# Performance work log

Measured on AMD Instinct MI355X. Metric: run time of the kernel, lower is better.

The kernel has to match this reference:

```python
import jax, jax.numpy as jnp
import numpy as np

MAX_NUM_CAPS = 10
NEG = -1e9

def _layernorm(x, g, b):
    m = x.mean(-1, keepdims=True)
    v = x.var(-1, keepdims=True)
    return (x - m) / jnp.sqrt(v + 1e-5) * g + b

def _gatv2(x, Wl, Wr, att, bias, adj):
    # x: [B,M,F]; Wl/Wr: [F,H*C]; att: [H,C]; adj: [B,M,M] bool, adj[b,i,j] = edge i->j
    B, M, F = x.shape
    H, C = att.shape
    xl = jnp.einsum('bmf,fhc->bmhc', x, Wl.reshape(F, H, C))  # source transform
    xr = jnp.einsum('bmf,fhc->bmhc', x, Wr.reshape(F, H, C))  # target transform
    # GATv2 score: att . leaky_relu(xl[i] + xr[j]) for edge (src=i, dst=j)
    z = jax.nn.leaky_relu(xl[:, :, None, :, :] + xr[:, None, :, :, :], 0.2)  # [B,i,j,H,C]
    e = jnp.einsum('bijhc,hc->bijh', z, att)
    e = jnp.where(adj[..., None], e, NEG)
    alpha = jax.nn.softmax(e, axis=1)  # softmax over incoming sources i per target j
    out = jnp.einsum('bijh,bihc->bjhc', alpha, xl)  # aggregate at targets
    return out.reshape(B, M, H * C) + bias

def setup_inputs() -> dict:
    key = jax.random.key(0)
    ks = jax.random.split(key, 16)
    B, N, T = 128, 16, 48
    Fm, H, C3 = 128, 4, 64
    s = 0.05
    inp = {
        'team_obs': jax.random.normal(ks[0], (B, N, 14), jnp.float32),
        'target_obs': jax.random.normal(ks[1], (B, T, 15), jnp.float32),
        'team_mask': jax.random.normal(ks[2], (B, 2, N), jnp.float32),
        'local_target_mask': jnp.ones((B, T + 1), jnp.float32),
        'W_emb': jax.random.normal(ks[3], (16, Fm), jnp.float32) * s,
        'b_emb': jnp.zeros((Fm,), jnp.float32),
        'Wl1': jax.random.normal(ks[4], (Fm, Fm), jnp.float32) * s,
        'Wr1': jax.random.normal(ks[5], (Fm, Fm), jnp.float32) * s,
        'att1': jax.random.normal(ks[6], (H, Fm // H), jnp.float32) * s,
        'b1': jnp.zeros((Fm,), jnp.float32),
        'Wl2': jax.random.normal(ks[7], (Fm, Fm), jnp.float32) * s,
        'Wr2': jax.random.normal(ks[8], (Fm, Fm), jnp.float32) * s,
        'att2': jax.random.normal(ks[9], (H, Fm // H), jnp.float32) * s,
        'b2': jnp.zeros((Fm,), jnp.float32),
        'Wl3': jax.random.normal(ks[10], (Fm, C3), jnp.float32) * s,
        'Wr3': jax.random.normal(ks[11], (Fm, C3), jnp.float32) * s,
        'att3': jax.random.normal(ks[12], (1, C3), jnp.float32) * s,
        'b3': jnp.zeros((C3,), jnp.float32),
        'ln1_g': jnp.ones((Fm,), jnp.float32),
        'ln1_b': jnp.zeros((Fm,), jnp.float32),
        'ln2_g': jnp.ones((Fm,), jnp.float32),
        'ln2_b': jnp.zeros((Fm,), jnp.float32),
    }
    return inp

def reference(team_obs, target_obs, team_mask, local_target_mask,
              W_emb, b_emb, Wl1, Wr1, att1, b1, Wl2, Wr2, att2, b2,
              Wl3, Wr3, att3, b3, ln1_g, ln1_b, ln2_g, ln2_b):
    B, N, _ = team_obs.shape
    team = jnp.concatenate([team_obs, jnp.zeros((B, N, 2), team_obs.dtype)], axis=2)
    tgt = target_obs[:, :, :-1]
    T = tgt.shape[1]
    tgt = jnp.concatenate([tgt[:, :, :2 + MAX_NUM_CAPS],
                           jnp.zeros((B, T, 2), tgt.dtype),
                           tgt[:, :, -2:]], axis=2)
    fin = jnp.concatenate([team, tgt], axis=1)  # [B, M, inp_dim]
    h = fin @ W_emb + b_emb  # [B, M, 128]
    imp_team = team_mask[:, 0] != -1e9          # [B, N]
    imp_tgt = local_target_mask[:, :-1] != 0.0  # [B, T]
    imp = jnp.concatenate([imp_team, imp_tgt], axis=1)  # [B, M]
    M = N + T
    eye = jnp.eye(M, dtype=bool)
    # edges among active nodes minus diagonal; PyG GATv2Conv add_self_loops=True re-adds self edges
    adj = (imp[:, :, None] & imp[:, None, :] & ~eye) | eye  # [B, M, M]
    out = jax.nn.relu(_layernorm(_gatv2(h, Wl1, Wr1, att1, b1, adj), ln1_g, ln1_b))
    out = jax.nn.relu(_layernorm(_gatv2(out, Wl2, Wr2, att2, b2, adj), ln2_g, ln2_b))
    out = _gatv2(out, Wl3, Wr3, att3, b3, adj)
    return out  # [B, M, out_dim]
```

## Files before the change

### kernel.cpp

```cpp
#include <hip/hip_runtime.h>

typedef unsigned short u16;
typedef unsigned int   u32;
typedef _Float16 h2  __attribute__((ext_vector_type(2)));
typedef __fp16   hw2 __attribute__((ext_vector_type(2)));
typedef __fp16   hw8 __attribute__((ext_vector_type(8)));
typedef float    f4  __attribute__((ext_vector_type(4)));

#define XS 136

static __device__ __forceinline__ h2 pk(float a, float b) {
    return __builtin_bit_cast(h2, __builtin_amdgcn_cvt_pkrtz(a, b));
}
static __device__ __forceinline__ float dot2(h2 a, h2 b, float c) {
    return __builtin_amdgcn_fdot2(__builtin_bit_cast(hw2, a),
                                  __builtin_bit_cast(hw2, b), c, false);
}
static __device__ __forceinline__ h2  b2h(u32 v) { return __builtin_bit_cast(h2, v); }
static __device__ __forceinline__ u32 h2u(h2 v)  { return __builtin_bit_cast(u32, v); }
static __device__ __forceinline__ h2  abs2(h2 v) { return b2h(h2u(v) & 0x7fff7fffu); }
static __device__ __forceinline__ u16 f2h(float f) { return __builtin_bit_cast(u16, (_Float16)f); }
static __device__ __forceinline__ float h2f(u16 v) { return (float)__builtin_bit_cast(_Float16, v); }
static __device__ __forceinline__ f4 mfma16(uint4 a, uint4 b, f4 c) {
    return __builtin_amdgcn_mfma_f32_16x16x32_f16(__builtin_bit_cast(hw8, a),
                                                  __builtin_bit_cast(hw8, b), c, 0, 0, 0);
}

__global__ void pack_weights(const float* __restrict__ Wl1, const float* __restrict__ Wr1,
                             const float* __restrict__ Wl2, const float* __restrict__ Wr2,
                             const float* __restrict__ Wl3, const float* __restrict__ Wr3,
                             u32* __restrict__ wpk)
{
    const int o = blockIdx.x * 256 + threadIdx.x;
    const float* src; u32* dst; int local; int N;
    if      (o < 8192)  { src = Wl1; dst = wpk;         local = o;         N = 128; }
    else if (o < 16384) { src = Wr1; dst = wpk + 8192;  local = o - 8192;  N = 128; }
    else if (o < 24576) { src = Wl2; dst = wpk + 16384; local = o - 16384; N = 128; }
    else if (o < 32768) { src = Wr2; dst = wpk + 24576; local = o - 24576; N = 128; }
    else if (o < 36864) { src = Wl3; dst = wpk + 32768; local = o - 32768; N = 64;  }
    else                { src = Wr3; dst = wpk + 36864; local = o - 36864; N = 64;  }
    const int i2   = local & 3;
    const int lane = (local >> 2) & 63;
    const int frag = local >> 8;
    const int kb   = frag & 3;
    const int nt   = frag >> 2;
    const int k0   = kb*32 + ((lane >> 4) << 3) + i2*2;
    const int n    = nt*16 + (lane & 15);
    dst[local] = h2u(pk(src[k0*N + n], src[(k0+1)*N + n]));
}

static __device__ __forceinline__ void gat_layer(
    int t, int w, int lane,
    const u32* __restrict__ wpkL, const u32* __restrict__ wpkR,
    const float* __restrict__ att, const float* __restrict__ bias,
    const float* __restrict__ lg, const float* __restrict__ lb,
    u16* sX, u16* sXl, uint4* sXrP, float* sAl, float* sPart, float* sL2, const float* sImp)
{
    {
        const int  mt  = w & 3;
        const bool isR = (w >= 4);
        const u32* wp  = isR ? wpkR : wpkL;
        const int  n15 = lane & 15;
        const int  qd  = lane >> 4;
        uint4 afr[4];
#pragma unroll
        for (int kb = 0; kb < 4; kb++)
            afr[kb] = *(const uint4*)&sX[(mt*16 + n15)*XS + kb*32 + (qd << 3)];
#pragma unroll
        for (int nt = 0; nt < 8; nt++) {
            f4 acc = {0.f, 0.f, 0.f, 0.f};
#pragma unroll
            for (int kb = 0; kb < 4; kb++) {
                uint4 bf = *(const uint4*)&wp[((nt*4 + kb)*64 + lane)*4];
                acc = mfma16(afr[kb], bf, acc);
            }
            const int n  = nt*16 + n15;
            const int mb = mt*16 + (qd << 2);
            if (!isR) {
#pragma unroll
                for (int r = 0; r < 4; r++) sXl[(mb + r)*XS + n] = f2h(acc[r]);
            } else {
                u16* xp = (u16*)sXrP;
#pragma unroll
                for (int r = 0; r < 4; r++)
                    xp[(((n >> 3)*64) + mb + r)*8 + (n & 7)] = f2h(acc[r]);
            }
        }
    }
    __syncthreads();

    const int h     = w & 3;
    const int ihalf = w >> 2;
    const int j     = lane;

    h2 a2[16];
#pragma unroll
    for (int q = 0; q < 16; q++) a2[q] = pk(att[h*32 + 2*q], att[h*32 + 2*q + 1]);

    if (w < 4) {
        const uint4* pr = (const uint4*)&sXl[lane*XS + h*32];
        float al = 0.f;
#pragma unroll
        for (int c4 = 0; c4 < 4; c4++) {
            uint4 v = pr[c4];
            al = dot2(b2h(v.x), a2[c4*4+0], al);
            al = dot2(b2h(v.y), a2[c4*4+1], al);
            al = dot2(b2h(v.z), a2[c4*4+2], al);
            al = dot2(b2h(v.w), a2[c4*4+3], al);
        }
        sAl[h*64 + lane] = al;
    }

    h2 xr2[16];
#pragma unroll
    for (int s = 0; s < 4; s++) {
        uint4 v = sXrP[(h*4 + s)*64 + j];
        xr2[s*4+0] = b2h(v.x); xr2[s*4+1] = b2h(v.y);
        xr2[s*4+2] = b2h(v.z); xr2[s*4+3] = b2h(v.w);
    }
    float Ar = 0.f;
#pragma unroll
    for (int q = 0; q < 16; q++) Ar = dot2(a2[q], xr2[q], Ar);
    const float impj = sImp[j];
    __syncthreads();

    float l = 0.f;
    h2 acc2[16];
#pragma unroll
    for (int q = 0; q < 16; q++) acc2[q] = b2h(0u);
    const int i0 = ihalf * 32;
#pragma unroll 4
    for (int ii = 0; ii < 32; ii++) {
        int i = i0 + ii;
        const uint4* pl = (const uint4*)&sXl[i*XS + h*32];
        uint4 v0 = pl[0], v1 = pl[1], v2 = pl[2], v3 = pl[3];
        h2 xl2[16];
        xl2[0] = b2h(v0.x); xl2[1] = b2h(v0.y); xl2[2]  = b2h(v0.z); xl2[3]  = b2h(v0.w);
        xl2[4] = b2h(v1.x); xl2[5] = b2h(v1.y); xl2[6]  = b2h(v1.z); xl2[7]  = b2h(v1.w);
        xl2[8] = b2h(v2.x); xl2[9] = b2h(v2.y); xl2[10] = b2h(v2.z); xl2[11] = b2h(v2.w);
        xl2[12]= b2h(v3.x); xl2[13]= b2h(v3.y); xl2[14] = b2h(v3.z); xl2[15] = b2h(v3.w);
        float S0 = 0.f, S1 = 0.f;
#pragma unroll
        for (int q = 0; q < 16; q += 2) {
            h2 t0 = abs2(xl2[q]   + xr2[q]);
            h2 t1 = abs2(xl2[q+1] + xr2[q+1]);
            S0 = dot2(a2[q],   t0, S0);
            S1 = dot2(a2[q+1], t1, S1);
        }
        float e  = 0.6f*(sAl[h*64 + i] + Ar) + 0.4f*(S0 + S1);
        float ad = (i == j) ? 1.f : impj * sImp[i];
        float p  = (ad != 0.f) ? __expf(e) : 0.f;
        l += p;
        h2 p2 = pk(p, p);
#pragma unroll
        for (int q = 0; q < 16; q++) acc2[q] += p2 * xl2[q];
    }

    u32* ov = (u32*)sX;
    if (w >= 4) {
        uint4* d4 = (uint4*)(ov + (h*64 + j)*16);
        uint4 o;
        o.x = h2u(acc2[0]);  o.y = h2u(acc2[1]);  o.z = h2u(acc2[2]);  o.w = h2u(acc2[3]);  d4[0] = o;
        o.x = h2u(acc2[4]);  o.y = h2u(acc2[5]);  o.z = h2u(acc2[6]);  o.w = h2u(acc2[7]);  d4[1] = o;
        o.x = h2u(acc2[8]);  o.y = h2u(acc2[9]);  o.z = h2u(acc2[10]); o.w = h2u(acc2[11]); d4[2] = o;
        o.x = h2u(acc2[12]); o.y = h2u(acc2[13]); o.z = h2u(acc2[14]); o.w = h2u(acc2[15]); d4[3] = o;
        sL2[h*64 + j] = l;
    }
    __syncthreads();

    float yv[32];
    if (w < 4) {
        const uint4* s4 = (const uint4*)(ov + (h*64 + j)*16);
        uint4 u0 = s4[0], u1 = s4[1], u2 = s4[2], u3 = s4[3];
        h2 oth[16];
        oth[0] = b2h(u0.x); oth[1] = b2h(u0.y); oth[2]  = b2h(u0.z); oth[3]  = b2h(u0.w);
        oth[4] = b2h(u1.x); oth[5] = b2h(u1.y); oth[6]  = b2h(u1.z); oth[7]  = b2h(u1.w);
        oth[8] = b2h(u2.x); oth[9] = b2h(u2.y); oth[10] = b2h(u2.z); oth[11] = b2h(u2.w);
        oth[12]= b2h(u3.x); oth[13]= b2h(u3.y); oth[14] = b2h(u3.z); oth[15] = b2h(u3.w);
        l += sL2[h*64 + j];
        const float rl = 1.f / l;
        float s1 = 0.f, s2v = 0.f;
#pragma unroll
        for (int q = 0; q < 16; q++) {
            h2 sum = acc2[q] + oth[q];
            float y0 = fmaf((float)sum[0], rl, bias[h*32 + 2*q]);
            float y1 = fmaf((float)sum[1], rl, bias[h*32 + 2*q + 1]);
            yv[2*q] = y0; yv[2*q+1] = y1;
            s1 += y0 + y1;
            s2v = fmaf(y0, y0, s2v);
            s2v = fmaf(y1, y1, s2v);
        }
        sPart[h*64 + j]       = s1;
        sPart[256 + h*64 + j] = s2v;
    }
    __syncthreads();

    if (w < 4) {
        float su = sPart[j] + sPart[64 + j] + sPart[128 + j] + sPart[192 + j];
        float sq = sPart[256 + j] + sPart[320 + j] + sPart[384 + j] + sPart[448 + j];
        const float mean = su * 0.0078125f;
        const float var  = sq * 0.0078125f - mean*mean;
        const float rstd = rsqrtf(var + 1e-5f);
        u32* xd = (u32*)&sX[j*XS + h*32];
#pragma unroll
        for (int q = 0; q < 16; q++) {
            int f0 = h*32 + 2*q;
            float v0 = fmaxf(fmaf((yv[2*q]   - mean)*rstd, lg[f0],   lb[f0]),   0.f);
            float v1 = fmaxf(fmaf((yv[2*q+1] - mean)*rstd, lg[f0+1], lb[f0+1]), 0.f);
            xd[q] = h2u(pk(v0, v1));
        }
    }
    __syncthreads();
}

__global__ void __launch_bounds__(512, 2) GNN_61040075210810_kernel(
    const float* __restrict__ team_obs, const float* __restrict__ target_obs,
    const float* __restrict__ team_mask, const float* __restrict__ local_target_mask,
    const float* __restrict__ W_emb, const float* __restrict__ b_emb,
    const float* __restrict__ att1, const float* __restrict__ b1,
    const float* __restrict__ att2, const float* __restrict__ b2,
    const float* __restrict__ att3, const float* __restrict__ b3,
    const float* __restrict__ ln1_g, const float* __restrict__ ln1_b,
    const float* __restrict__ ln2_g, const float* __restrict__ ln2_b,
    const u32* __restrict__ wpk,
    float* __restrict__ out)
{
    __shared__ __align__(16) u16   sX  [64*XS];
    __shared__ __align__(16) u16   sXl [64*XS];
    __shared__ __align__(16) uint4 sXrP[1024];
    __shared__ float sFin[1024];
    __shared__ float sAl [256];
    __shared__ float sPart[512];
    __shared__ float sL2 [256];
    __shared__ float sImp[64];

    const int t    = threadIdx.x;
    const int w    = t >> 6;
    const int lane = t & 63;
    const int b    = blockIdx.x;

    if (t < 64) {
        float im;
        if (t < 16) im = (team_mask[b*32 + t] != -1000000000.0f) ? 1.f : 0.f;
        else        im = (local_target_mask[b*49 + (t-16)] != 0.0f) ? 1.f : 0.f;
        sImp[t] = im;
    }
    for (int ee = t; ee < 1024; ee += 512) {
        int m = ee >> 4, k = ee & 15;
        float v = 0.f;
        if (m < 16) {
            if (k < 14) v = team_obs[(b*16 + m)*14 + k];
        } else {
            const float* tg = target_obs + (size_t)(b*48 + (m-16))*15;
            if      (k < 12)  v = tg[k];
            else if (k == 14) v = tg[12];
            else if (k == 15) v = tg[13];
        }
        sFin[m*16 + k] = v;
    }
    __syncthreads();

    {
        const int f = t & 127;
        const int g = t >> 7;
        float wreg[16];
#pragma unroll
        for (int k = 0; k < 16; k++) wreg[k] = W_emb[k*128 + f];
        const float bf = b_emb[f];
#pragma unroll
        for (int mm = 0; mm < 16; mm++) {
            int m = g*16 + mm;
            const float4* pf = (const float4*)&sFin[m*16];
            float4 f0 = pf[0], f1 = pf[1], f2 = pf[2], f3 = pf[3];
            float acc = bf;
            acc = fmaf(f0.x, wreg[0],  acc); acc = fmaf(f0.y, wreg[1],  acc);
            acc = fmaf(f0.z, wreg[2],  acc); acc = fmaf(f0.w, wreg[3],  acc);
            acc = fmaf(f1.x, wreg[4],  acc); acc = fmaf(f1.y, wreg[5],  acc);
            acc = fmaf(f1.z, wreg[6],  acc); acc = fmaf(f1.w, wreg[7],  acc);
            acc = fmaf(f2.x, wreg[8],  acc); acc = fmaf(f2.y, wreg[9],  acc);
            acc = fmaf(f2.z, wreg[10], acc); acc = fmaf(f2.w, wreg[11], acc);
            acc = fmaf(f3.x, wreg[12], acc); acc = fmaf(f3.y, wreg[13], acc);
            acc = fmaf(f3.z, wreg[14], acc); acc = fmaf(f3.w, wreg[15], acc);
            sX[m*XS + f] = f2h(acc);
        }
    }
    __syncthreads();

    gat_layer(t, w, lane, wpk,         wpk + 8192,  att1, b1, ln1_g, ln1_b,
              sX, sXl, sXrP, sAl, sPart, sL2, sImp);
    gat_layer(t, w, lane, wpk + 16384, wpk + 24576, att2, b2, ln2_g, ln2_b,
              sX, sXl, sXrP, sAl, sPart, sL2, sImp);

    {
        const int  mt  = w & 3;
        const bool isR = (w >= 4);
        const u32* wp  = isR ? (wpk + 36864) : (wpk + 32768);
        const int  n15 = lane & 15;
        const int  qd  = lane >> 4;
        uint4 afr[4];
#pragma unroll
        for (int kb = 0; kb < 4; kb++)
            afr[kb] = *(const uint4*)&sX[(mt*16 + n15)*XS + kb*32 + (qd << 3)];
#pragma unroll
        for (int nt = 0; nt < 4; nt++) {
            f4 acc = {0.f, 0.f, 0.f, 0.f};
#pragma unroll
            for (int kb = 0; kb < 4; kb++) {
                uint4 bf = *(const uint4*)&wp[((nt*4 + kb)*64 + lane)*4];
                acc = mfma16(afr[kb], bf, acc);
            }
            const int n  = nt*16 + n15;
            const int mb = mt*16 + (qd << 2);
            if (!isR) {
#pragma unroll
                for (int r = 0; r < 4; r++) sXl[(mb + r)*XS + n] = f2h(acc[r]);
            } else {
                u16* xp = (u16*)sXrP;
#pragma unroll
                for (int r = 0; r < 4; r++)
                    xp[(((n >> 3)*64) + mb + r)*8 + (n & 7)] = f2h(acc[r]);
            }
        }
    }
    __syncthreads();

    {
        h2 a2l[4];
#pragma unroll
        for (int q = 0; q < 4; q++) a2l[q] = pk(att3[w*8 + 2*q], att3[w*8 + 2*q + 1]);
        uint4 v = *(const uint4*)&sXl[lane*XS + w*8];
        float al = 0.f;
        al = dot2(b2h(v.x), a2l[0], al);
        al = dot2(b2h(v.y), a2l[1], al);
        al = dot2(b2h(v.z), a2l[2], al);
        al = dot2(b2h(v.w), a2l[3], al);
        sPart[w*64 + lane] = al;
    }
    __syncthreads();
    if (t < 64) {
        sAl[t] = ((sPart[t] + sPart[64+t]) + (sPart[128+t] + sPart[192+t]))
               + ((sPart[256+t] + sPart[320+t]) + (sPart[384+t] + sPart[448+t]));
    }
    __syncthreads();

    const int j = lane;
    u16* sE = (u16*)sX;

    {
        h2 a3[32], xr3[32];
#pragma unroll
        for (int q = 0; q < 32; q++) a3[q] = pk(att3[2*q], att3[2*q + 1]);
#pragma unroll
        for (int s = 0; s < 8; s++) {
            uint4 v = sXrP[s*64 + j];
            xr3[s*4+0] = b2h(v.x); xr3[s*4+1] = b2h(v.y);
            xr3[s*4+2] = b2h(v.z); xr3[s*4+3] = b2h(v.w);
        }
        float Ar = 0.f;
#pragma unroll
        for (int q = 0; q < 32; q++) Ar = dot2(a3[q], xr3[q], Ar);
        const float impj = sImp[j];
        const int i0 = w*8;
        for (int ii = 0; ii < 8; ii++) {
            int i = i0 + ii;
            const uint4* pl = (const uint4*)&sXl[i*XS];
            float S0 = 0.f, S1 = 0.f;
#pragma unroll
            for (int c4 = 0; c4 < 8; c4++) {
                uint4 v = pl[c4];
                S0 = dot2(a3[c4*4+0], abs2(b2h(v.x) + xr3[c4*4+0]), S0);
                S1 = dot2(a3[c4*4+1], abs2(b2h(v.y) + xr3[c4*4+1]), S1);
                S0 = dot2(a3[c4*4+2], abs2(b2h(v.z) + xr3[c4*4+2]), S0);
                S1 = dot2(a3[c4*4+3], abs2(b2h(v.w) + xr3[c4*4+3]), S1);
            }
            float e  = 0.6f*(sAl[i] + Ar) + 0.4f*(S0 + S1);
            float ad = (i == j) ? 1.f : impj * sImp[i];
            e = (ad != 0.f) ? e : -60000.0f;
            sE[i*64 + j] = f2h(e);
        }
    }
    __syncthreads();

    {
        const int c0 = w*8;
        h2 acc2[4];
#pragma unroll
        for (int q = 0; q < 4; q++) acc2[q] = b2h(0u);
        float l = 0.f;
        for (int i = 0; i < 64; i++) {
            float p = __expf(h2f(sE[i*64 + j]));
            l += p;
            h2 p2 = pk(p, p);
            uint4 v = *(const uint4*)&sXl[i*XS + c0];
            acc2[0] += p2 * b2h(v.x);
            acc2[1] += p2 * b2h(v.y);
            acc2[2] += p2 * b2h(v.z);
            acc2[3] += p2 * b2h(v.w);
        }
        const float rl = 1.f / l;
        float o[8];
#pragma unroll
        for (int q = 0; q < 4; q++) {
            o[2*q]   = fmaf((float)acc2[q][0], rl, b3[c0 + 2*q]);
            o[2*q+1] = fmaf((float)acc2[q][1], rl, b3[c0 + 2*q + 1]);
        }
        float4* po = (float4*)(out + (size_t)b*4096 + j*64 + c0);
        po[0] = *(const float4*)&o[0];
        po[1] = *(const float4*)&o[4];
    }
}

extern "C" void kernel_launch(void* const* d_in, const int* in_sizes, int n_in,
                              void* d_out, int out_size, void* d_ws, size_t ws_size,
                              hipStream_t stream) {
    (void)in_sizes; (void)n_in; (void)ws_size; (void)out_size;
    const float* team_obs          = (const float*)d_in[0];
    const float* target_obs        = (const float*)d_in[1];
    const float* team_mask         = (const float*)d_in[2];
    const float* local_target_mask = (const float*)d_in[3];
    const float* W_emb             = (const float*)d_in[4];
    const float* b_emb             = (const float*)d_in[5];
    const float* Wl1               = (const float*)d_in[6];
    const float* Wr1               = (const float*)d_in[7];
    const float* att1              = (const float*)d_in[8];
    const float* b1                = (const float*)d_in[9];
    const float* Wl2               = (const float*)d_in[10];
    const float* Wr2               = (const float*)d_in[11];
    const float* att2              = (const float*)d_in[12];
    const float* b2                = (const float*)d_in[13];
    const float* Wl3               = (const float*)d_in[14];
    const float* Wr3               = (const float*)d_in[15];
    const float* att3              = (const float*)d_in[16];
    const float* b3                = (const float*)d_in[17];
    const float* ln1_g             = (const float*)d_in[18];
    const float* ln1_b             = (const float*)d_in[19];
    const float* ln2_g             = (const float*)d_in[20];
    const float* ln2_b             = (const float*)d_in[21];
    float* out = (float*)d_out;
    u32*   wpk = (u32*)d_ws;

    pack_weights<<<dim3(160), dim3(256), 0, stream>>>(Wl1, Wr1, Wl2, Wr2, Wl3, Wr3, wpk);
    GNN_61040075210810_kernel<<<dim3(128), dim3(512), 0, stream>>>(
        team_obs, target_obs, team_mask, local_target_mask, W_emb, b_emb,
        att1, b1, att2, b2, att3, b3, ln1_g, ln1_b, ln2_g, ln2_b, wpk, out);
}
```

Before: 144.8 us.

## Split fused GNN kernel into per-layer kernels over two target halves

Replaces the single fused kernel (one block per batch, 128 blocks) with three per-layer kernels, each launched with 256 blocks, where every block handles half of the target nodes. Each block recomputes the full node projections for its batch, splits the source loop across lane halves and combines the partial sums with xor-32 shuffles, then writes intermediate activations to global memory (output buffer and workspace). The aim is to fill more of the GPU's compute units at batch 128. The cost is duplicated matmul work, extra kernel launches and a global round trip between layers.

```diff
diff --git a/kernel.cpp b/kernel.cpp
--- a/kernel.cpp
+++ b/kernel.cpp
@@ -24,6 +24,9 @@
 static __device__ __forceinline__ f4 mfma16(uint4 a, uint4 b, f4 c) {
     return __builtin_amdgcn_mfma_f32_16x16x32_f16(__builtin_bit_cast(hw8, a),
                                                   __builtin_bit_cast(hw8, b), c, 0, 0, 0);
+}
+static __device__ __forceinline__ h2 shflx32(h2 v) {
+    return b2h((u32)__shfl_xor((int)h2u(v), 32));
 }
 
 __global__ void pack_weights(const float* __restrict__ Wl1, const float* __restrict__ Wr1,
@@ -49,49 +52,63 @@
     dst[local] = h2u(pk(src[k0*N + n], src[(k0+1)*N + n]));
 }
 
-static __device__ __forceinline__ void gat_layer(
-    int t, int w, int lane,
+static __device__ __forceinline__ void compute_imp(int t, int b,
+    const float* __restrict__ team_mask, const float* __restrict__ ltm, float* sImp)
+{
+    if (t < 64) {
+        float im;
+        if (t < 16) im = (team_mask[b*32 + t] != -1000000000.0f) ? 1.f : 0.f;
+        else        im = (ltm[b*49 + (t-16)] != 0.0f) ? 1.f : 0.f;
+        sImp[t] = im;
+    }
+}
+
+static __device__ __forceinline__ void matmul128(int w, int lane,
     const u32* __restrict__ wpkL, const u32* __restrict__ wpkR,
+    const u16* sX, u16* sXl, uint4* sXrP)
+{
+    const int  mt  = w & 3;
+    const bool isR = (w >= 4);
+    const u32* wp  = isR ? wpkR : wpkL;
+    const int  n15 = lane & 15;
+    const int  qd  = lane >> 4;
+    uint4 afr[4];
+#pragma unroll
+    for (int kb = 0; kb < 4; kb++)
+        afr[kb] = *(const uint4*)&sX[(mt*16 + n15)*XS + kb*32 + (qd << 3)];
+#pragma unroll
+    for (int nt = 0; nt < 8; nt++) {
+        f4 acc = {0.f, 0.f, 0.f, 0.f};
+#pragma unroll
+        for (int kb = 0; kb < 4; kb++) {
+            uint4 bf = *(const uint4*)&wp[((nt*4 + kb)*64 + lane)*4];
+            acc = mfma16(afr[kb], bf, acc);
+        }
+        const int n  = nt*16 + n15;
+        const int mb = mt*16 + (qd << 2);
+        if (!isR) {
+#pragma unroll
+            for (int r = 0; r < 4; r++) sXl[(mb + r)*XS + n] = f2h(acc[r]);
+        } else {
+            u16* xp = (u16*)sXrP;
+#pragma unroll
+            for (int r = 0; r < 4; r++)
+                xp[(((n >> 3)*64) + mb + r)*8 + (n & 7)] = f2h(acc[r]);
+        }
+    }
+}
+
+static __device__ __forceinline__ void attn_ln(int t, int w, int lane, int b, int jh,
     const float* __restrict__ att, const float* __restrict__ bias,
     const float* __restrict__ lg, const float* __restrict__ lb,
-    u16* sX, u16* sXl, uint4* sXrP, float* sAl, float* sPart, float* sL2, const float* sImp)
-{
-    {
-        const int  mt  = w & 3;
-        const bool isR = (w >= 4);
-        const u32* wp  = isR ? wpkR : wpkL;
-        const int  n15 = lane & 15;
-        const int  qd  = lane >> 4;
-        uint4 afr[4];
-#pragma unroll
-        for (int kb = 0; kb < 4; kb++)
-            afr[kb] = *(const uint4*)&sX[(mt*16 + n15)*XS + kb*32 + (qd << 3)];
-#pragma unroll
-        for (int nt = 0; nt < 8; nt++) {
-            f4 acc = {0.f, 0.f, 0.f, 0.f};
-#pragma unroll
-            for (int kb = 0; kb < 4; kb++) {
-                uint4 bf = *(const uint4*)&wp[((nt*4 + kb)*64 + lane)*4];
-                acc = mfma16(afr[kb], bf, acc);
-            }
-            const int n  = nt*16 + n15;
-            const int mb = mt*16 + (qd << 2);
-            if (!isR) {
-#pragma unroll
-                for (int r = 0; r < 4; r++) sXl[(mb + r)*XS + n] = f2h(acc[r]);
-            } else {
-                u16* xp = (u16*)sXrP;
-#pragma unroll
-                for (int r = 0; r < 4; r++)
-                    xp[(((n >> 3)*64) + mb + r)*8 + (n & 7)] = f2h(acc[r]);
-            }
-        }
-    }
-    __syncthreads();
-
-    const int h     = w & 3;
-    const int ihalf = w >> 2;
-    const int j     = lane;
+    u16* sX, const u16* sXl, const uint4* sXrP,
+    float* sAl, float* sPart, float* sL2, const float* sImp, u32* __restrict__ gxOut)
+{
+    const int h  = w & 3;
+    const int ih = w >> 2;
+    const int jj = lane & 31;
+    const int is = lane >> 5;
+    const int j  = jh*32 + jj;
 
     h2 a2[16];
 #pragma unroll
@@ -128,9 +145,9 @@
     h2 acc2[16];
 #pragma unroll
     for (int q = 0; q < 16; q++) acc2[q] = b2h(0u);
-    const int i0 = ihalf * 32;
+    const int i0 = ih*32 + is*16;
 #pragma unroll 4
-    for (int ii = 0; ii < 32; ii++) {
+    for (int ii = 0; ii < 16; ii++) {
         int i = i0 + ii;
         const uint4* pl = (const uint4*)&sXl[i*XS + h*32];
         uint4 v0 = pl[0], v1 = pl[1], v2 = pl[2], v3 = pl[3];
@@ -156,28 +173,32 @@
         for (int q = 0; q < 16; q++) acc2[q] += p2 * xl2[q];
     }
 
+    l += __shfl_xor(l, 32);
+#pragma unroll
+    for (int q = 0; q < 16; q++) acc2[q] = acc2[q] + shflx32(acc2[q]);
+
     u32* ov = (u32*)sX;
-    if (w >= 4) {
-        uint4* d4 = (uint4*)(ov + (h*64 + j)*16);
+    if (w >= 4 && lane < 32) {
+        uint4* d4 = (uint4*)(ov + (h*32 + jj)*20);
         uint4 o;
         o.x = h2u(acc2[0]);  o.y = h2u(acc2[1]);  o.z = h2u(acc2[2]);  o.w = h2u(acc2[3]);  d4[0] = o;
         o.x = h2u(acc2[4]);  o.y = h2u(acc2[5]);  o.z = h2u(acc2[6]);  o.w = h2u(acc2[7]);  d4[1] = o;
         o.x = h2u(acc2[8]);  o.y = h2u(acc2[9]);  o.z = h2u(acc2[10]); o.w = h2u(acc2[11]); d4[2] = o;
         o.x = h2u(acc2[12]); o.y = h2u(acc2[13]); o.z = h2u(acc2[14]); o.w = h2u(acc2[15]); d4[3] = o;
-        sL2[h*64 + j] = l;
+        sL2[h*32 + jj] = l;
     }
     __syncthreads();
 
     float yv[32];
-    if (w < 4) {
-        const uint4* s4 = (const uint4*)(ov + (h*64 + j)*16);
+    if (w < 4 && lane < 32) {
+        const uint4* s4 = (const uint4*)(ov + (h*32 + jj)*20);
         uint4 u0 = s4[0], u1 = s4[1], u2 = s4[2], u3 = s4[3];
         h2 oth[16];
         oth[0] = b2h(u0.x); oth[1] = b2h(u0.y); oth[2]  = b2h(u0.z); oth[3]  = b2h(u0.w);
         oth[4] = b2h(u1.x); oth[5] = b2h(u1.y); oth[6]  = b2h(u1.z); oth[7]  = b2h(u1.w);
         oth[8] = b2h(u2.x); oth[9] = b2h(u2.y); oth[10] = b2h(u2.z); oth[11] = b2h(u2.w);
         oth[12]= b2h(u3.x); oth[13]= b2h(u3.y); oth[14] = b2h(u3.z); oth[15] = b2h(u3.w);
-        l += sL2[h*64 + j];
+        l += sL2[h*32 + jj];
         const float rl = 1.f / l;
         float s1 = 0.f, s2v = 0.f;
 #pragma unroll
@@ -190,61 +211,57 @@
             s2v = fmaf(y0, y0, s2v);
             s2v = fmaf(y1, y1, s2v);
         }
-        sPart[h*64 + j]       = s1;
-        sPart[256 + h*64 + j] = s2v;
-    }
-    __syncthreads();
-
-    if (w < 4) {
-        float su = sPart[j] + sPart[64 + j] + sPart[128 + j] + sPart[192 + j];
-        float sq = sPart[256 + j] + sPart[320 + j] + sPart[384 + j] + sPart[448 + j];
+        sPart[h*32 + jj]       = s1;
+        sPart[128 + h*32 + jj] = s2v;
+    }
+    __syncthreads();
+
+    if (w < 4 && lane < 32) {
+        float su = sPart[jj] + sPart[32 + jj] + sPart[64 + jj] + sPart[96 + jj];
+        float sq = sPart[128 + jj] + sPart[160 + jj] + sPart[192 + jj] + sPart[224 + jj];
         const float mean = su * 0.0078125f;
         const float var  = sq * 0.0078125f - mean*mean;
         const float rstd = rsqrtf(var + 1e-5f);
-        u32* xd = (u32*)&sX[j*XS + h*32];
 #pragma unroll
         for (int q = 0; q < 16; q++) {
             int f0 = h*32 + 2*q;
             float v0 = fmaxf(fmaf((yv[2*q]   - mean)*rstd, lg[f0],   lb[f0]),   0.f);
             float v1 = fmaxf(fmaf((yv[2*q+1] - mean)*rstd, lg[f0+1], lb[f0+1]), 0.f);
-            xd[q] = h2u(pk(v0, v1));
-        }
-    }
-    __syncthreads();
-}
-
-__global__ void __launch_bounds__(512, 2) GNN_61040075210810_kernel(
+            ov[(h*32 + jj)*20 + q] = h2u(pk(v0, v1));
+        }
+    }
+    __syncthreads();
+
+    for (int r = t; r < 2048; r += 512) {
+        int nj = r >> 6, c = r & 63, hh = c >> 4, qq = c & 15;
+        gxOut[(size_t)b*4096 + (size_t)(jh*32 + nj)*64 + c] = ov[(hh*32 + nj)*20 + qq];
+    }
+}
+
+__global__ void __launch_bounds__(512, 1) gnn_layer1(
     const float* __restrict__ team_obs, const float* __restrict__ target_obs,
-    const float* __restrict__ team_mask, const float* __restrict__ local_target_mask,
+    const float* __restrict__ team_mask, const float* __restrict__ ltm,
     const float* __restrict__ W_emb, const float* __restrict__ b_emb,
     const float* __restrict__ att1, const float* __restrict__ b1,
-    const float* __restrict__ att2, const float* __restrict__ b2,
-    const float* __restrict__ att3, const float* __restrict__ b3,
     const float* __restrict__ ln1_g, const float* __restrict__ ln1_b,
-    const float* __restrict__ ln2_g, const float* __restrict__ ln2_b,
-    const u32* __restrict__ wpk,
-    float* __restrict__ out)
+    const u32* __restrict__ wpk, u32* __restrict__ gx1)
 {
     __shared__ __align__(16) u16   sX  [64*XS];
     __shared__ __align__(16) u16   sXl [64*XS];
     __shared__ __align__(16) uint4 sXrP[1024];
     __shared__ float sFin[1024];
     __shared__ float sAl [256];
-    __shared__ float sPart[512];
-    __shared__ float sL2 [256];
+    __shared__ float sPart[256];
+    __shared__ float sL2 [128];
     __shared__ float sImp[64];
 
     const int t    = threadIdx.x;
     const int w    = t >> 6;
     const int lane = t & 63;
-    const int b    = blockIdx.x;
-
-    if (t < 64) {
-        float im;
-        if (t < 16) im = (team_mask[b*32 + t] != -1000000000.0f) ? 1.f : 0.f;
-        else        im = (local_target_mask[b*49 + (t-16)] != 0.0f) ? 1.f : 0.f;
-        sImp[t] = im;
-    }
+    const int b    = blockIdx.x >> 1;
+    const int jh   = blockIdx.x & 1;
+
+    compute_imp(t, b, team_mask, ltm, sImp);
     for (int ee = t; ee < 1024; ee += 512) {
         int m = ee >> 4, k = ee & 15;
         float v = 0.f;
@@ -286,10 +303,74 @@
     }
     __syncthreads();
 
-    gat_layer(t, w, lane, wpk,         wpk + 8192,  att1, b1, ln1_g, ln1_b,
-              sX, sXl, sXrP, sAl, sPart, sL2, sImp);
-    gat_layer(t, w, lane, wpk + 16384, wpk + 24576, att2, b2, ln2_g, ln2_b,
-              sX, sXl, sXrP, sAl, sPart, sL2, sImp);
+    matmul128(w, lane, wpk, wpk + 8192, sX, sXl, sXrP);
+    __syncthreads();
+    attn_ln(t, w, lane, b, jh, att1, b1, ln1_g, ln1_b,
+            sX, sXl, sXrP, sAl, sPart, sL2, sImp, gx1);
+}
+
+__global__ void __launch_bounds__(512, 1) gnn_layer2(
+    const float* __restrict__ team_mask, const float* __restrict__ ltm,
+    const float* __restrict__ att2, const float* __restrict__ b2,
+    const float* __restrict__ ln2_g, const float* __restrict__ ln2_b,
+    const u32* __restrict__ wpk, const u32* __restrict__ gxIn, u32* __restrict__ gxOut)
+{
+    __shared__ __align__(16) u16   sX  [64*XS];
+    __shared__ __align__(16) u16   sXl [64*XS];
+    __shared__ __align__(16) uint4 sXrP[1024];
+    __shared__ float sAl [256];
+    __shared__ float sPart[256];
+    __shared__ float sL2 [128];
+    __shared__ float sImp[64];
+
+    const int t    = threadIdx.x;
+    const int w    = t >> 6;
+    const int lane = t & 63;
+    const int b    = blockIdx.x >> 1;
+    const int jh   = blockIdx.x & 1;
+
+    compute_imp(t, b, team_mask, ltm, sImp);
+    const uint4* gin = (const uint4*)(gxIn + (size_t)b*4096);
+    for (int r = t; r < 1024; r += 512) {
+        uint4 v = gin[r];
+        int m = r >> 4, seg = r & 15;
+        *(uint4*)&sX[m*XS + seg*8] = v;
+    }
+    __syncthreads();
+
+    matmul128(w, lane, wpk + 16384, wpk + 24576, sX, sXl, sXrP);
+    __syncthreads();
+    attn_ln(t, w, lane, b, jh, att2, b2, ln2_g, ln2_b,
+            sX, sXl, sXrP, sAl, sPart, sL2, sImp, gxOut);
+}
+
+__global__ void __launch_bounds__(512, 1) gnn_layer3(
+    const float* __restrict__ team_mask, const float* __restrict__ ltm,
+    const float* __restrict__ att3, const float* __restrict__ b3,
+    const u32* __restrict__ wpk, const u32* __restrict__ gxIn, float* __restrict__ out)
+{
+    __shared__ __align__(16) u16   sX  [64*XS];
+    __shared__ __align__(16) u16   sXl [64*XS];
+    __shared__ __align__(16) uint4 sXrP[512];
+    __shared__ float sAl [64];
+    __shared__ float sPart[512];
+    __shared__ float sImp[64];
+    __shared__ u16   sE  [64*32];
+
+    const int t    = threadIdx.x;
+    const int w    = t >> 6;
+    const int lane = t & 63;
+    const int b    = blockIdx.x >> 1;
+    const int jh   = blockIdx.x & 1;
+
+    compute_imp(t, b, team_mask, ltm, sImp);
+    const uint4* gin = (const uint4*)(gxIn + (size_t)b*4096);
+    for (int r = t; r < 1024; r += 512) {
+        uint4 v = gin[r];
+        int m = r >> 4, seg = r & 15;
+        *(uint4*)&sX[m*XS + seg*8] = v;
+    }
+    __syncthreads();
 
     {
         const int  mt  = w & 3;
@@ -343,8 +424,9 @@
     }
     __syncthreads();
 
-    const int j = lane;
-    u16* sE = (u16*)sX;
+    const int jj = lane & 31;
+    const int is = lane >> 5;
+    const int j  = jh*32 + jj;
 
     {
         h2 a3[32], xr3[32];
@@ -360,9 +442,9 @@
 #pragma unroll
         for (int q = 0; q < 32; q++) Ar = dot2(a3[q], xr3[q], Ar);
         const float impj = sImp[j];
-        const int i0 = w*8;
-        for (int ii = 0; ii < 8; ii++) {
-            int i = i0 + ii;
+        const int ib = (w*2 + is)*4;
+        for (int ii = 0; ii < 4; ii++) {
+            int i = ib + ii;
             const uint4* pl = (const uint4*)&sXl[i*XS];
             float S0 = 0.f, S1 = 0.f;
 #pragma unroll
@@ -376,7 +458,7 @@
             float e  = 0.6f*(sAl[i] + Ar) + 0.4f*(S0 + S1);
             float ad = (i == j) ? 1.f : impj * sImp[i];
             e = (ad != 0.f) ? e : -60000.0f;
-            sE[i*64 + j] = f2h(e);
+            sE[i*32 + jj] = f2h(e);
         }
     }
     __syncthreads();
@@ -387,8 +469,9 @@
 #pragma unroll
         for (int q = 0; q < 4; q++) acc2[q] = b2h(0u);
         float l = 0.f;
-        for (int i = 0; i < 64; i++) {
-            float p = __expf(h2f(sE[i*64 + j]));
+        for (int k = 0; k < 32; k++) {
+            int i = is*32 + k;
+            float p = __expf(h2f(sE[i*32 + jj]));
             l += p;
             h2 p2 = pk(p, p);
             uint4 v = *(const uint4*)&sXl[i*XS + c0];
@@ -397,16 +480,21 @@
             acc2[2] += p2 * b2h(v.z);
             acc2[3] += p2 * b2h(v.w);
         }
-        const float rl = 1.f / l;
-        float o[8];
-#pragma unroll
-        for (int q = 0; q < 4; q++) {
-            o[2*q]   = fmaf((float)acc2[q][0], rl, b3[c0 + 2*q]);
-            o[2*q+1] = fmaf((float)acc2[q][1], rl, b3[c0 + 2*q + 1]);
-        }
-        float4* po = (float4*)(out + (size_t)b*4096 + j*64 + c0);
-        po[0] = *(const float4*)&o[0];
-        po[1] = *(const float4*)&o[4];
+        l += __shfl_xor(l, 32);
+#pragma unroll
+        for (int q = 0; q < 4; q++) acc2[q] = acc2[q] + shflx32(acc2[q]);
+        if (is == 0) {
+            const float rl = 1.f / l;
+            float o[8];
+#pragma unroll
+            for (int q = 0; q < 4; q++) {
+                o[2*q]   = fmaf((float)acc2[q][0], rl, b3[c0 + 2*q]);
+                o[2*q+1] = fmaf((float)acc2[q][1], rl, b3[c0 + 2*q + 1]);
+            }
+            float4* po = (float4*)(out + (size_t)b*4096 + (size_t)j*64 + c0);
+            po[0] = *(const float4*)&o[0];
+            po[1] = *(const float4*)&o[4];
+        }
     }
 }
 
@@ -437,10 +525,17 @@
     const float* ln2_g             = (const float*)d_in[20];
     const float* ln2_b             = (const float*)d_in[21];
     float* out = (float*)d_out;
-    u32*   wpk = (u32*)d_ws;
+
+    u32* wpk = (u32*)d_ws;
+    u32* gx2 = (u32*)d_ws + 40960;
+    u32* gx1 = (u32*)d_out;
 
     pack_weights<<<dim3(160), dim3(256), 0, stream>>>(Wl1, Wr1, Wl2, Wr2, Wl3, Wr3, wpk);
-    GNN_61040075210810_kernel<<<dim3(128), dim3(512), 0, stream>>>(
+    gnn_layer1<<<dim3(256), dim3(512), 0, stream>>>(
         team_obs, target_obs, team_mask, local_target_mask, W_emb, b_emb,
-        att1, b1, att2, b2, att3, b3, ln1_g, ln1_b, ln2_g, ln2_b, wpk, out);
-}
+        att1, b1, ln1_g, ln1_b, wpk, gx1);
+    gnn_layer2<<<dim3(256), dim3(512), 0, stream>>>(
+        team_mask, local_target_mask, att2, b2, ln2_g, ln2_b, wpk, gx1, gx2);
+    gnn_layer3<<<dim3(256), dim3(512), 0, stream>>>(
+        team_mask, local_target_mask, att3, b3, wpk, gx2, out);
+}
```

Result: faster. 138.6 us (-4.3%).
